# Kernel tuning notes

Hardware: AMD Instinct MI355X
Metric: run time of the kernel (lower is better)

The kernel has to match this reference:

```python
import jax, jax.numpy as jnp
import numpy as np

H = 512   # hidden_dim
B = 1024  # batch
D = 256   # history length


def setup_inputs() -> dict:
    key = jax.random.key(0)
    k1, k2, k3, k4, k5, k6 = jax.random.split(key, 6)
    return {
        "h_tilde": jax.random.normal(k1, (B, H), dtype=jnp.float32),
        "c_t": jax.random.normal(k2, (B, H), dtype=jnp.float32),
        "h_history": jax.random.normal(k3, (B, D, H), dtype=jnp.float32),
        # learned parameters (nn.Linear stores weight as [out, in]; y = x @ W.T)
        "Waq": jax.random.normal(k4, (H, 2 * H), dtype=jnp.float32) * (1.0 / np.sqrt(2 * H)),
        "Wah": jax.random.normal(k5, (H, H), dtype=jnp.float32) * (1.0 / np.sqrt(H)),
        "ba": jnp.zeros((H,), dtype=jnp.float32),
        "v_t": jax.random.normal(k6, (H,), dtype=jnp.float32),
    }


def reference(h_tilde, c_t, h_history, Waq, Wah, ba, v_t):
    # q_t = [h_tilde ; c_t] -> [B, 2H]; project to [B, H]
    q_t = jnp.concatenate([h_tilde, c_t], axis=1)
    q_proj = q_t @ Waq.T                         # [B, H]
    h_proj = jnp.einsum('bdh,gh->bdg', h_history, Wah)  # [B, D, H]
    # broadcast add + tanh: the large [B, D, H] intermediate
    score_pre = jnp.tanh(q_proj[:, None, :] + h_proj + ba)
    alpha_unscaled = jnp.einsum('bdh,h->bd', score_pre, v_t)  # [B, D]
    alpha = jax.nn.softmax(alpha_unscaled, axis=1)            # [B, D]
    e_t = jnp.einsum('bd,bdh->bh', alpha, h_history)          # [B, H]
    return (e_t, alpha)
```

## Files before the change

### kernel.cpp

```cpp
#include <hip/hip_runtime.h>
#include <hip/hip_bf16.h>

#define HDIM 512
#define BDIM 1024
#define DDIM 256
#define MTOT (BDIM * DDIM)

typedef _Float16 half8 __attribute__((ext_vector_type(8)));
typedef float f32x4 __attribute__((ext_vector_type(4)));

__device__ __forceinline__ float ftanh(float x) {
    float e = __expf(2.0f * x);
    return 1.0f - 2.0f / (e + 1.0f);
}

__device__ __forceinline__ void gl_lds16(const _Float16* src, _Float16* dst) {
    __builtin_amdgcn_global_load_lds((const __attribute__((address_space(1))) void*)src,
                                     (__attribute__((address_space(3))) void*)dst,
                                     16, 0, 0);
}

__global__ __launch_bounds__(256) void k_convertW(const float* __restrict__ Wah,
                                                  _Float16* __restrict__ W16) {
    int n = blockIdx.x * 256 + threadIdx.x;
    int chunk = n >> 10, r = n & 1023;
    int kb = r >> 6, kp = (r >> 4) & 3, g = r & 15;
    const float* src = Wah + (size_t)(chunk * 16 + g) * 512 + kb * 32 + kp * 8;
    float4 v0 = *(const float4*)src;
    float4 v1 = *(const float4*)(src + 4);
    half8 h;
    h[0] = (_Float16)v0.x; h[1] = (_Float16)v0.y; h[2] = (_Float16)v0.z; h[3] = (_Float16)v0.w;
    h[4] = (_Float16)v1.x; h[5] = (_Float16)v1.y; h[6] = (_Float16)v1.z; h[7] = (_Float16)v1.w;
    *(half8*)&W16[(size_t)n * 8] = h;
}

__global__ __launch_bounds__(256) void k_qproj(const float* __restrict__ h_tilde,
                                               const float* __restrict__ c_t,
                                               const float* __restrict__ Waq,
                                               const float* __restrict__ ba,
                                               float* __restrict__ qb) {
    __shared__ float qs[4][1024];
    int t = threadIdx.x;
    int b0 = blockIdx.x * 4;
    #pragma unroll
    for (int p = 0; p < 4; p++) {
        int f4 = t + p * 256;
        int e = f4 * 4;
        int row = e >> 10, k = e & 1023;
        float4 v;
        if (k < 512) v = *(const float4*)&h_tilde[(b0 + row) * 512 + k];
        else         v = *(const float4*)&c_t[(b0 + row) * 512 + k - 512];
        *(float4*)&qs[row][k] = v;
    }
    __syncthreads();
    int g0 = t, g1 = t + 256;
    float acc0[4] = {0.f, 0.f, 0.f, 0.f};
    float acc1[4] = {0.f, 0.f, 0.f, 0.f};
    const float4* w0p = (const float4*)&Waq[(size_t)g0 * 1024];
    const float4* w1p = (const float4*)&Waq[(size_t)g1 * 1024];
    #pragma unroll 4
    for (int k4 = 0; k4 < 256; k4++) {
        float4 w0 = w0p[k4];
        float4 w1 = w1p[k4];
        #pragma unroll
        for (int bb = 0; bb < 4; bb++) {
            float4 q = *(const float4*)&qs[bb][k4 * 4];
            acc0[bb] += q.x * w0.x + q.y * w0.y + q.z * w0.z + q.w * w0.w;
            acc1[bb] += q.x * w1.x + q.y * w1.y + q.z * w1.z + q.w * w1.w;
        }
    }
    #pragma unroll
    for (int bb = 0; bb < 4; bb++) {
        qb[(b0 + bb) * 512 + g0] = acc0[bb] + ba[g0];
        qb[(b0 + bb) * 512 + g1] = acc1[bb] + ba[g1];
    }
}

__global__ __launch_bounds__(256, 4) void k_logits(const float* __restrict__ hist,
                                                   const float* __restrict__ qb,
                                                   const _Float16* __restrict__ W16,
                                                   const float* __restrict__ v_t,
                                                   float* __restrict__ logits) {
    __shared__ _Float16 Wb[2][8192];
    __shared__ float qbs[512];
    __shared__ float vsh[512];

    int t = threadIdx.x;
    int w = t >> 6, lane = t & 63, l15 = lane & 15, l4 = lane >> 4;
    size_t m_base = (size_t)blockIdx.x * 64;
    int b = blockIdx.x >> 2;

    qbs[t] = qb[b * 512 + t];
    qbs[t + 256] = qb[b * 512 + 256 + t];
    vsh[t] = v_t[t];
    vsh[t + 256] = v_t[256 + t];

    #pragma unroll
    for (int sg = 0; sg < 4; sg++)
        gl_lds16(W16 + ((size_t)(w * 4 + sg) * 64 + lane) * 8,
                 &Wb[0][(w * 4 + sg) * 512]);

    half8 afr[16];
    const float* xb = hist + (m_base + w * 16 + l15) * 512 + l4 * 8;
    #pragma unroll
    for (int kb = 0; kb < 16; kb++) {
        const float* p = xb + kb * 32;
        float4 v0 = *(const float4*)p;
        float4 v1 = *(const float4*)(p + 4);
        half8 h;
        h[0] = (_Float16)v0.x; h[1] = (_Float16)v0.y; h[2] = (_Float16)v0.z; h[3] = (_Float16)v0.w;
        h[4] = (_Float16)v1.x; h[5] = (_Float16)v1.y; h[6] = (_Float16)v1.z; h[7] = (_Float16)v1.w;
        afr[kb] = h;
    }

    float S[4] = {0.f, 0.f, 0.f, 0.f};

    __syncthreads();

    const _Float16* bufbase0 = &Wb[0][lane * 8];
    const _Float16* bufbase1 = &Wb[1][lane * 8];

    for (int c = 0; c < 32; c++) {
        int cur = c & 1;
        if (c < 31) {
            const _Float16* wc = W16 + (size_t)(c + 1) * 8192;
            _Float16* wd = Wb[cur ^ 1];
            #pragma unroll
            for (int sg = 0; sg < 4; sg++)
                gl_lds16(wc + ((size_t)(w * 4 + sg) * 64 + lane) * 8,
                         &wd[(w * 4 + sg) * 512]);
        }
        const _Float16* bufp = cur ? bufbase1 : bufbase0;
        f32x4 tac = (f32x4){0.f, 0.f, 0.f, 0.f};
        __builtin_amdgcn_s_setprio(1);
        #pragma unroll
        for (int kb = 0; kb < 16; kb++) {
            half8 bf = *(const half8*)(bufp + kb * 512);
            tac = __builtin_amdgcn_mfma_f32_16x16x32_f16(afr[kb], bf, tac, 0, 0, 0);
        }
        __builtin_amdgcn_s_setprio(0);
        float qv = qbs[c * 16 + l15];
        float vv = vsh[c * 16 + l15];
        #pragma unroll
        for (int j = 0; j < 4; j++)
            S[j] += ftanh(tac[j] + qv) * vv;
        __syncthreads();
    }

    #pragma unroll
    for (int j = 0; j < 4; j++) {
        float s = S[j];
        s += __shfl_xor(s, 1, 64);
        s += __shfl_xor(s, 2, 64);
        s += __shfl_xor(s, 4, 64);
        s += __shfl_xor(s, 8, 64);
        if (l15 == 0)
            logits[m_base + w * 16 + l4 * 4 + j] = s;
    }
}

__global__ __launch_bounds__(256) void k_softmax_et(const float* __restrict__ hist,
                                                    const float* __restrict__ logits,
                                                    float* __restrict__ out) {
    __shared__ float as_[256];
    __shared__ float wred[4];
    __shared__ float ered[512];
    int b = blockIdx.x, t = threadIdx.x;
    float l = logits[b * 256 + t];
    float m = l;
    m = fmaxf(m, __shfl_xor(m, 1, 64));
    m = fmaxf(m, __shfl_xor(m, 2, 64));
    m = fmaxf(m, __shfl_xor(m, 4, 64));
    m = fmaxf(m, __shfl_xor(m, 8, 64));
    m = fmaxf(m, __shfl_xor(m, 16, 64));
    m = fmaxf(m, __shfl_xor(m, 32, 64));
    if ((t & 63) == 0) wred[t >> 6] = m;
    __syncthreads();
    m = fmaxf(fmaxf(wred[0], wred[1]), fmaxf(wred[2], wred[3]));
    float e = __expf(l - m);
    float s = e;
    s += __shfl_xor(s, 1, 64);
    s += __shfl_xor(s, 2, 64);
    s += __shfl_xor(s, 4, 64);
    s += __shfl_xor(s, 8, 64);
    s += __shfl_xor(s, 16, 64);
    s += __shfl_xor(s, 32, 64);
    __syncthreads();
    if ((t & 63) == 0) wred[t >> 6] = s;
    __syncthreads();
    s = wred[0] + wred[1] + wred[2] + wred[3];
    float a = e / s;
    out[BDIM * HDIM + b * 256 + t] = a;
    as_[t] = a;
    __syncthreads();
    int c4 = (t & 127) * 4;
    int dp = t >> 7;
    float e0 = 0.f, e1 = 0.f, e2 = 0.f, e3 = 0.f;
    const float* hb = hist + (size_t)b * 256 * 512 + c4;
    #pragma unroll 4
    for (int d = dp; d < 256; d += 2) {
        float al = as_[d];
        float4 h = *(const float4*)&hb[(size_t)d * 512];
        e0 += al * h.x; e1 += al * h.y; e2 += al * h.z; e3 += al * h.w;
    }
    if (dp) {
        float4 v; v.x = e0; v.y = e1; v.z = e2; v.w = e3;
        *(float4*)&ered[c4] = v;
    }
    __syncthreads();
    if (!dp) {
        float4 p = *(const float4*)&ered[c4];
        float4 r; r.x = e0 + p.x; r.y = e1 + p.y; r.z = e2 + p.z; r.w = e3 + p.w;
        *(float4*)&out[b * 512 + c4] = r;
    }
}

extern "C" void kernel_launch(void* const* d_in, const int* in_sizes, int n_in,
                              void* d_out, int out_size, void* d_ws, size_t ws_size,
                              hipStream_t stream) {
    const float* h_tilde = (const float*)d_in[0];
    const float* c_t     = (const float*)d_in[1];
    const float* hist    = (const float*)d_in[2];
    const float* Waq     = (const float*)d_in[3];
    const float* Wah     = (const float*)d_in[4];
    const float* ba      = (const float*)d_in[5];
    const float* v_t     = (const float*)d_in[6];
    float* out = (float*)d_out;

    char* ws = (char*)d_ws;
    float*    qb     = (float*)ws;
    _Float16* W16    = (_Float16*)(ws + (2u << 20));
    float*    logits = (float*)(ws + (3u << 20));

    k_convertW<<<128, 256, 0, stream>>>(Wah, W16);
    k_qproj<<<256, 256, 0, stream>>>(h_tilde, c_t, Waq, ba, qb);
    k_logits<<<4096, 256, 0, stream>>>(hist, qb, W16, v_t, logits);
    k_softmax_et<<<1024, 256, 0, stream>>>(hist, logits, out);
}
```

Measured before the change: 414.4 us.

## Fuse softmax-weighted history sum into logits kernel with online-softmax partials

The logits kernel now computes per-block softmax partials (max, sum) and the exp-weighted partial sums of the history rows, using the fp16 fragments it already holds in registers. A small combine kernel merges the four partials per batch row into alpha and e_t. This removes the second full read of h_history. It adds shuffle reductions and LDS traffic to the logits kernel, and e_t is now computed from fp16-rounded history values.

```diff
diff --git a/kernel.cpp b/kernel.cpp
--- a/kernel.cpp
+++ b/kernel.cpp
@@ -80,15 +80,19 @@
                                                    const float* __restrict__ qb,
                                                    const _Float16* __restrict__ W16,
                                                    const float* __restrict__ v_t,
-                                                   float* __restrict__ logits) {
+                                                   float* __restrict__ logits,
+                                                   float* __restrict__ eparts,
+                                                   float* __restrict__ ms) {
     __shared__ _Float16 Wb[2][8192];
     __shared__ float qbs[512];
     __shared__ float vsh[512];
+    __shared__ float lsh[64];
 
     int t = threadIdx.x;
     int w = t >> 6, lane = t & 63, l15 = lane & 15, l4 = lane >> 4;
-    size_t m_base = (size_t)blockIdx.x * 64;
-    int b = blockIdx.x >> 2;
+    int bx = blockIdx.x;
+    size_t m_base = (size_t)bx * 64;
+    int b = bx >> 2;
 
     qbs[t] = qb[b * 512 + t];
     qbs[t + 256] = qb[b * 512 + 256 + t];
@@ -154,65 +158,79 @@
         s += __shfl_xor(s, 2, 64);
         s += __shfl_xor(s, 4, 64);
         s += __shfl_xor(s, 8, 64);
-        if (l15 == 0)
+        if (l15 == 0) {
             logits[m_base + w * 16 + l4 * 4 + j] = s;
-    }
-}
-
-__global__ __launch_bounds__(256) void k_softmax_et(const float* __restrict__ hist,
-                                                    const float* __restrict__ logits,
-                                                    float* __restrict__ out) {
-    __shared__ float as_[256];
-    __shared__ float wred[4];
-    __shared__ float ered[512];
+            lsh[w * 16 + l4 * 4 + j] = s;
+        }
+    }
+    __syncthreads();
+
+    float lv = lsh[lane];
+    float mb = lv;
+    mb = fmaxf(mb, __shfl_xor(mb, 1, 64));
+    mb = fmaxf(mb, __shfl_xor(mb, 2, 64));
+    mb = fmaxf(mb, __shfl_xor(mb, 4, 64));
+    mb = fmaxf(mb, __shfl_xor(mb, 8, 64));
+    mb = fmaxf(mb, __shfl_xor(mb, 16, 64));
+    mb = fmaxf(mb, __shfl_xor(mb, 32, 64));
+    float eb = __expf(lv - mb);
+    float sb = eb;
+    sb += __shfl_xor(sb, 1, 64);
+    sb += __shfl_xor(sb, 2, 64);
+    sb += __shfl_xor(sb, 4, 64);
+    sb += __shfl_xor(sb, 8, 64);
+    sb += __shfl_xor(sb, 16, 64);
+    sb += __shfl_xor(sb, 32, 64);
+
+    float coef = __expf(lsh[w * 16 + l15] - mb);
+    float* ews = (float*)Wb;
+    #pragma unroll
+    for (int kb = 0; kb < 16; kb++) {
+        float ep[8];
+        half8 x = afr[kb];
+        #pragma unroll
+        for (int e2 = 0; e2 < 8; e2++) ep[e2] = coef * (float)x[e2];
+        #pragma unroll
+        for (int e2 = 0; e2 < 8; e2++) {
+            ep[e2] += __shfl_xor(ep[e2], 1, 64);
+            ep[e2] += __shfl_xor(ep[e2], 2, 64);
+            ep[e2] += __shfl_xor(ep[e2], 4, 64);
+            ep[e2] += __shfl_xor(ep[e2], 8, 64);
+        }
+        if (l15 == 0) {
+            #pragma unroll
+            for (int e2 = 0; e2 < 8; e2++)
+                ews[w * 512 + kb * 32 + l4 * 8 + e2] = ep[e2];
+        }
+    }
+    __syncthreads();
+    float v0 = ews[t] + ews[512 + t] + ews[1024 + t] + ews[1536 + t];
+    float v1 = ews[256 + t] + ews[768 + t] + ews[1280 + t] + ews[1792 + t];
+    eparts[(size_t)bx * 512 + t] = v0;
+    eparts[(size_t)bx * 512 + 256 + t] = v1;
+    if (t == 0) { ms[bx * 2] = mb; ms[bx * 2 + 1] = sb; }
+}
+
+__global__ __launch_bounds__(256) void k_comb(const float* __restrict__ logits,
+                                              const float* __restrict__ eparts,
+                                              const float* __restrict__ ms,
+                                              float* __restrict__ out) {
     int b = blockIdx.x, t = threadIdx.x;
+    float m0 = ms[(4 * b + 0) * 2], s0 = ms[(4 * b + 0) * 2 + 1];
+    float m1 = ms[(4 * b + 1) * 2], s1 = ms[(4 * b + 1) * 2 + 1];
+    float m2 = ms[(4 * b + 2) * 2], s2 = ms[(4 * b + 2) * 2 + 1];
+    float m3 = ms[(4 * b + 3) * 2], s3 = ms[(4 * b + 3) * 2 + 1];
+    float m = fmaxf(fmaxf(m0, m1), fmaxf(m2, m3));
+    float w0 = __expf(m0 - m), w1 = __expf(m1 - m);
+    float w2 = __expf(m2 - m), w3 = __expf(m3 - m);
+    float Sb = w0 * s0 + w1 * s1 + w2 * s2 + w3 * s3;
     float l = logits[b * 256 + t];
-    float m = l;
-    m = fmaxf(m, __shfl_xor(m, 1, 64));
-    m = fmaxf(m, __shfl_xor(m, 2, 64));
-    m = fmaxf(m, __shfl_xor(m, 4, 64));
-    m = fmaxf(m, __shfl_xor(m, 8, 64));
-    m = fmaxf(m, __shfl_xor(m, 16, 64));
-    m = fmaxf(m, __shfl_xor(m, 32, 64));
-    if ((t & 63) == 0) wred[t >> 6] = m;
-    __syncthreads();
-    m = fmaxf(fmaxf(wred[0], wred[1]), fmaxf(wred[2], wred[3]));
-    float e = __expf(l - m);
-    float s = e;
-    s += __shfl_xor(s, 1, 64);
-    s += __shfl_xor(s, 2, 64);
-    s += __shfl_xor(s, 4, 64);
-    s += __shfl_xor(s, 8, 64);
-    s += __shfl_xor(s, 16, 64);
-    s += __shfl_xor(s, 32, 64);
-    __syncthreads();
-    if ((t & 63) == 0) wred[t >> 6] = s;
-    __syncthreads();
-    s = wred[0] + wred[1] + wred[2] + wred[3];
-    float a = e / s;
-    out[BDIM * HDIM + b * 256 + t] = a;
-    as_[t] = a;
-    __syncthreads();
-    int c4 = (t & 127) * 4;
-    int dp = t >> 7;
-    float e0 = 0.f, e1 = 0.f, e2 = 0.f, e3 = 0.f;
-    const float* hb = hist + (size_t)b * 256 * 512 + c4;
-    #pragma unroll 4
-    for (int d = dp; d < 256; d += 2) {
-        float al = as_[d];
-        float4 h = *(const float4*)&hb[(size_t)d * 512];
-        e0 += al * h.x; e1 += al * h.y; e2 += al * h.z; e3 += al * h.w;
-    }
-    if (dp) {
-        float4 v; v.x = e0; v.y = e1; v.z = e2; v.w = e3;
-        *(float4*)&ered[c4] = v;
-    }
-    __syncthreads();
-    if (!dp) {
-        float4 p = *(const float4*)&ered[c4];
-        float4 r; r.x = e0 + p.x; r.y = e1 + p.y; r.z = e2 + p.z; r.w = e3 + p.w;
-        *(float4*)&out[b * 512 + c4] = r;
-    }
+    out[BDIM * HDIM + b * 256 + t] = __expf(l - m) / Sb;
+    const float* ep = eparts + (size_t)(4 * b) * 512;
+    float a0 = w0 * ep[t] + w1 * ep[512 + t] + w2 * ep[1024 + t] + w3 * ep[1536 + t];
+    float a1 = w0 * ep[256 + t] + w1 * ep[768 + t] + w2 * ep[1280 + t] + w3 * ep[1792 + t];
+    out[b * 512 + t] = a0 / Sb;
+    out[b * 512 + 256 + t] = a1 / Sb;
 }
 
 extern "C" void kernel_launch(void* const* d_in, const int* in_sizes, int n_in,
@@ -231,9 +249,11 @@
     float*    qb     = (float*)ws;
     _Float16* W16    = (_Float16*)(ws + (2u << 20));
     float*    logits = (float*)(ws + (3u << 20));
+    float*    eparts = (float*)(ws + (4u << 20));
+    float*    ms     = (float*)(ws + (12u << 20));
 
     k_convertW<<<128, 256, 0, stream>>>(Wah, W16);
     k_qproj<<<256, 256, 0, stream>>>(h_tilde, c_t, Waq, ba, qb);
-    k_logits<<<4096, 256, 0, stream>>>(hist, qb, W16, v_t, logits);
-    k_softmax_et<<<1024, 256, 0, stream>>>(hist, logits, out);
-}
+    k_logits<<<4096, 256, 0, stream>>>(hist, qb, W16, v_t, logits, eparts, ms);
+    k_comb<<<1024, 256, 0, stream>>>(logits, eparts, ms, out);
+}
```

Result: faster. 391.7 us (-5.5%).
